# Performance work log

Measured on AMD Instinct MI355X. Metric: run time of the kernel, lower is better.

## Reference

```python
import jax, jax.numpy as jnp
import numpy as np

B, S, DIN, DOUT = 4, 2048, 2048, 8192


def setup_inputs() -> dict:
    key = jax.random.key(0)
    kx, kw = jax.random.split(key)
    x = jax.random.normal(kx, (B, S, DIN), dtype=jnp.float32)
    # match torch init: uniform(-bound, bound), bound = sqrt(3) * 0.5 * in_features**-0.5
    bound = (3.0 ** 0.5) * 0.5 * DIN ** (-0.5)
    weight = jax.random.uniform(kw, (DOUT, DIN), dtype=jnp.float32, minval=-bound, maxval=bound)
    return {"x": x, "weight": weight}


def _rms_norm(x):
    # F.rms_norm with no weight: eps defaults to finfo(dtype).eps
    eps = jnp.finfo(x.dtype).eps
    return x * jax.lax.rsqrt(jnp.mean(x * x, axis=-1, keepdims=True) + eps)


def _act_quant(xn):
    # per-token int8 symmetric quant/dequant
    scale = 127.0 / jnp.maximum(jnp.max(jnp.abs(xn), axis=-1, keepdims=True), 1e-5)
    return jnp.clip(jnp.round(xn * scale), -128.0, 127.0) / scale


def _weight_quant(w):
    # ternary weight quant/dequant with global abs-mean scale
    scale = 1.0 / jnp.maximum(jnp.mean(jnp.abs(w)), 1e-5)
    return jnp.clip(jnp.round(w * scale), -1.0, 1.0) / scale


def reference(x, weight):
    xn = _rms_norm(x)
    # STE: forward uses quantized values, gradient flows through xn / weight
    x_q = xn + jax.lax.stop_gradient(_act_quant(xn) - xn)
    w_q = weight + jax.lax.stop_gradient(_weight_quant(weight) - weight)
    # F.linear: x @ w.T  -> [B, S, DOUT]
    return jnp.einsum('bsd,od->bso', x_q, w_q)
```

## Files before the change

### kernel.cpp

```cpp
#include <hip/hip_runtime.h>

typedef unsigned short u16;
typedef unsigned int u32;
typedef int i32x4 __attribute__((ext_vector_type(4)));
typedef float f32x4 __attribute__((ext_vector_type(4)));

#define DIN 2048
#define DOUT 8192
#define MROWS 8192
#define NELEM_W (8192 * 2048)
#define NT 16

#define WS_PART 0
#define WS_WFAC 16384
#define WS_ROWFAC 16640
#define WS_XQ 49408
#define WS_WQ (49408 + 16777216)

__global__ void k_wabs(const float* __restrict__ w, double* __restrict__ part) {
    const float4* w4 = (const float4*)w;
    const unsigned t = threadIdx.x, b = blockIdx.x;
    float s = 0.f;
    for (unsigned i = b * 256u + t; i < (NELEM_W / 4); i += 2048u * 256u) {
        float4 v = w4[i];
        s += fabsf(v.x) + fabsf(v.y) + fabsf(v.z) + fabsf(v.w);
    }
    double d = (double)s;
    #pragma unroll
    for (int o = 32; o; o >>= 1) d += __shfl_down(d, o);
    __shared__ double red[4];
    if ((t & 63u) == 0u) red[t >> 6] = d;
    __syncthreads();
    if (t == 0) part[b] = red[0] + red[1] + red[2] + red[3];
}

__global__ void k_wfin(const double* __restrict__ part, float* __restrict__ wfac) {
    const int t = threadIdx.x;
    double s = 0.0;
    #pragma unroll
    for (int j = 0; j < 8; ++j) s += part[t + j * 256];
    #pragma unroll
    for (int o = 32; o; o >>= 1) s += __shfl_down(s, o);
    __shared__ double red[4];
    if ((t & 63) == 0) red[t >> 6] = s;
    __syncthreads();
    if (t == 0) {
        double mean = (red[0] + red[1] + red[2] + red[3]) * (1.0 / (double)NELEM_W);
        *wfac = fmaxf((float)mean, 1e-5f);
    }
}

__global__ void k_wquant(const float* __restrict__ w, const float* __restrict__ wfac,
                         u32* __restrict__ wq) {
    const float scale = 1.0f / *wfac;
    const float4* w4 = (const float4*)w;
    for (unsigned i = blockIdx.x * 256u + threadIdx.x; i < (NELEM_W / 4); i += 2048u * 256u) {
        float4 v = w4[i];
        int q0 = (int)fminf(fmaxf(rintf(v.x * scale), -1.f), 1.f);
        int q1 = (int)fminf(fmaxf(rintf(v.y * scale), -1.f), 1.f);
        int q2 = (int)fminf(fmaxf(rintf(v.z * scale), -1.f), 1.f);
        int q3 = (int)fminf(fmaxf(rintf(v.w * scale), -1.f), 1.f);
        wq[i] = (u32)(q0 & 255) | ((u32)(q1 & 255) << 8) |
                ((u32)(q2 & 255) << 16) | ((u32)(q3 & 255) << 24);
    }
}

__global__ void k_act(const float* __restrict__ x, u32* __restrict__ xq,
                      float* __restrict__ rowfac) {
    const int row = blockIdx.x, t = threadIdx.x;
    const float4* xr = (const float4*)(x + (size_t)row * DIN);
    float4 v0 = xr[t], v1 = xr[t + 256];
    float ss = v0.x * v0.x + v0.y * v0.y + v0.z * v0.z + v0.w * v0.w
             + v1.x * v1.x + v1.y * v1.y + v1.z * v1.z + v1.w * v1.w;
    __shared__ float red[4];
    #pragma unroll
    for (int o = 32; o; o >>= 1) ss += __shfl_down(ss, o);
    if ((t & 63) == 0) red[t >> 6] = ss;
    __syncthreads();
    ss = red[0] + red[1] + red[2] + red[3];
    const float r = 1.0f / sqrtf(ss * (1.0f / DIN) + 1.1920929e-7f);
    float xn[8] = {v0.x * r, v0.y * r, v0.z * r, v0.w * r,
                   v1.x * r, v1.y * r, v1.z * r, v1.w * r};
    float am = 0.f;
    #pragma unroll
    for (int j = 0; j < 8; ++j) am = fmaxf(am, fabsf(xn[j]));
    __syncthreads();
    #pragma unroll
    for (int o = 32; o; o >>= 1) am = fmaxf(am, __shfl_down(am, o));
    if ((t & 63) == 0) red[t >> 6] = am;
    __syncthreads();
    am = fmaxf(fmaxf(red[0], red[1]), fmaxf(red[2], red[3]));
    const float amc = fmaxf(am, 1e-5f);
    const float s = 127.0f / amc;
    int q[8];
    #pragma unroll
    for (int j = 0; j < 8; ++j)
        q[j] = (int)fminf(fmaxf(rintf(xn[j] * s), -128.f), 127.f);
    u32* xo = xq + (size_t)row * (DIN / 4);
    xo[t] = (u32)(q[0] & 255) | ((u32)(q[1] & 255) << 8) |
            ((u32)(q[2] & 255) << 16) | ((u32)(q[3] & 255) << 24);
    xo[t + 256] = (u32)(q[4] & 255) | ((u32)(q[5] & 255) << 8) |
                  ((u32)(q[6] & 255) << 16) | ((u32)(q[7] & 255) << 24);
    if (t == 0) rowfac[row] = amc * (1.0f / 127.0f);
}


#define STAGE(gbase, opOff, tt, kh) do {                                          \
    _Pragma("unroll")                                                             \
    for (int j_ = 0; j_ < 2; ++j_) {                                              \
        const int seg_ = w * 2 + j_;                                              \
        const int row_ = seg_ * 16 + (l >> 2);                                    \
        const int sc_ = (l & 3) ^ ((l >> 3) & 3);                                 \
        const char* src_ = (gbase) + (size_t)row_ * DIN + (tt) * 128 + (kh) * 64 + sc_ * 16; \
        __builtin_amdgcn_global_load_lds(                                         \
            (const __attribute__((address_space(1))) void*)src_,                  \
            (__attribute__((address_space(3))) void*)(smb + (opOff) + ((tt) & 1) * 32768 + (kh) * 16384 + seg_ * 1024), \
            16, 0, 0);                                                            \
    }                                                                             \
} while (0)

#define PHASE_MFMA(MBASE)                                                         \
    __builtin_amdgcn_s_barrier();                                                 \
    __builtin_amdgcn_s_setprio(1);                                                \
    _Pragma("unroll")                                                             \
    for (int i = 0; i < 4; ++i)                                                   \
        _Pragma("unroll")                                                         \
        for (int n = 0; n < 4; ++n)                                               \
            acc[(MBASE) + i][n] = __builtin_amdgcn_mfma_i32_16x16x64_i8(          \
                afr[i], bfr[n], acc[(MBASE) + i][n], 0, 0, 0);                    \
    __builtin_amdgcn_s_setprio(0);                                                \
    __builtin_amdgcn_s_barrier();

__launch_bounds__(512, 2)
__global__ void k_gemm(const char* __restrict__ A, const char* __restrict__ Bw,
                       const float* __restrict__ rowfac, const float* __restrict__ wfac,
                       float* __restrict__ out) {
    __shared__ __attribute__((aligned(16))) char smb[131072];

    const int t = threadIdx.x;
    const int l = t & 63, w = t >> 6;
    const int wm = w >> 2, wn = w & 3;
    const int lr = l & 15, lc = l >> 4;
    const int laneF = lr * 64 + ((lc ^ ((lr >> 1) & 3)) * 16);

    const int bid = blockIdx.x;
    const int wg = (bid & 7) * 128 + (bid >> 3);
    const int bm = wg >> 5, bn = wg & 31;

    const char* Ab = A + (size_t)(bm * 256) * DIN;
    const char* Bb = Bw + (size_t)(bn * 256) * DIN;

    i32x4 acc[8][4] = {};

    STAGE(Ab, 0, 0, 0);
    STAGE(Bb, 65536, 0, 0);
    STAGE(Ab, 0, 0, 1);
    STAGE(Bb, 65536, 0, 1);
    asm volatile("s_waitcnt vmcnt(4)" ::: "memory");
    __builtin_amdgcn_s_barrier();

    for (int kt = 0; kt < NT; ++kt) {
        const int AB = (kt & 1) * 32768;
        const bool more = (kt < NT - 1);
        const char* aBase = smb + AB;
        const char* bBase = smb + 65536 + AB;
        i32x4 afr[4], bfr[4];

        #pragma unroll
        for (int n = 0; n < 4; ++n)
            bfr[n] = *(const i32x4*)(bBase + (wn * 64 + n * 16) * 64 + laneF);
        #pragma unroll
        for (int i = 0; i < 4; ++i)
            afr[i] = *(const i32x4*)(aBase + (wm * 128 + i * 16) * 64 + laneF);
        if (more) STAGE(Ab, 0, kt + 1, 0);
        PHASE_MFMA(0)

        #pragma unroll
        for (int i = 0; i < 4; ++i)
            afr[i] = *(const i32x4*)(aBase + (wm * 128 + (4 + i) * 16) * 64 + laneF);
        if (more) {
            STAGE(Bb, 65536, kt + 1, 0);
            asm volatile("s_waitcnt vmcnt(4)" ::: "memory");
        } else {
            asm volatile("s_waitcnt vmcnt(0)" ::: "memory");
        }
        PHASE_MFMA(4)

        #pragma unroll
        for (int n = 0; n < 4; ++n)
            bfr[n] = *(const i32x4*)(bBase + 16384 + (wn * 64 + n * 16) * 64 + laneF);
        #pragma unroll
        for (int i = 0; i < 4; ++i)
            afr[i] = *(const i32x4*)(aBase + 16384 + (wm * 128 + i * 16) * 64 + laneF);
        if (more) STAGE(Ab, 0, kt + 1, 1);
        PHASE_MFMA(0)

        #pragma unroll
        for (int i = 0; i < 4; ++i)
            afr[i] = *(const i32x4*)(aBase + 16384 + (wm * 128 + (4 + i) * 16) * 64 + laneF);
        if (more) {
            STAGE(Bb, 65536, kt + 1, 1);
            asm volatile("s_waitcnt vmcnt(4)" ::: "memory");
        }
        PHASE_MFMA(4)
    }

    const float wf = *wfac;
    const int c0 = bn * 256 + wn * 64 + lr;
    #pragma unroll
    for (int m = 0; m < 8; ++m) {
        #pragma unroll
        for (int r = 0; r < 4; ++r) {
            const int grow = bm * 256 + wm * 128 + m * 16 + lc * 4 + r;
            const float s = rowfac[grow] * wf;
            const size_t ob = (size_t)grow * DOUT + c0;
            #pragma unroll
            for (int n = 0; n < 4; ++n)
                out[ob + n * 16] = (float)acc[m][n][r] * s;
        }
    }
}

extern "C" void kernel_launch(void* const* d_in, const int* in_sizes, int n_in,
                              void* d_out, int out_size, void* d_ws, size_t ws_size,
                              hipStream_t stream) {
    const float* x = (const float*)d_in[0];
    const float* wt = (const float*)d_in[1];
    float* out = (float*)d_out;
    char* ws = (char*)d_ws;

    double* part = (double*)(ws + WS_PART);
    float* wfac = (float*)(ws + WS_WFAC);
    float* rowfac = (float*)(ws + WS_ROWFAC);
    u32* xq = (u32*)(ws + WS_XQ);
    u32* wq = (u32*)(ws + WS_WQ);

    k_wabs<<<2048, 256, 0, stream>>>(wt, part);
    k_wfin<<<1, 256, 0, stream>>>(part, wfac);
    k_wquant<<<2048, 256, 0, stream>>>(wt, wfac, wq);
    k_act<<<8192, 256, 0, stream>>>(x, xq, rowfac);
    k_gemm<<<1024, 512, 0, stream>>>((const char*)xq, (const char*)wq, rowfac, wfac, out);
}
```

Before: 207.6 us.

## Restructure GEMM mainloop to full-tile double buffering and fuse quant kernels

The int8 GEMM main loop now stages a whole 128-wide K tile for A and B per step, using a new 128-byte-row XOR-swizzled LDS layout. It reads all fragments into registers before issuing 64 MFMAs, so one vmcnt(0)+barrier gate per K tile replaces the four barrier pairs per tile of the old phased loop. The weight-quant and activation-quant kernels are merged into one launch with block-index dispatch, removing a launch and letting the two run concurrently. In exchange, register pressure rises with the doubled fragment arrays, and waiting on vmcnt(0) per tile may expose load latency that the finer phasing used to hide.

```diff
diff --git a/kernel.cpp b/kernel.cpp
--- a/kernel.cpp
+++ b/kernel.cpp
@@ -3,13 +3,11 @@
 typedef unsigned short u16;
 typedef unsigned int u32;
 typedef int i32x4 __attribute__((ext_vector_type(4)));
-typedef float f32x4 __attribute__((ext_vector_type(4)));
 
 #define DIN 2048
 #define DOUT 8192
 #define MROWS 8192
 #define NELEM_W (8192 * 2048)
-#define NT 16
 
 #define WS_PART 0
 #define WS_WFAC 16384
@@ -50,24 +48,25 @@
     }
 }
 
-__global__ void k_wquant(const float* __restrict__ w, const float* __restrict__ wfac,
-                         u32* __restrict__ wq) {
-    const float scale = 1.0f / *wfac;
-    const float4* w4 = (const float4*)w;
-    for (unsigned i = blockIdx.x * 256u + threadIdx.x; i < (NELEM_W / 4); i += 2048u * 256u) {
-        float4 v = w4[i];
-        int q0 = (int)fminf(fmaxf(rintf(v.x * scale), -1.f), 1.f);
-        int q1 = (int)fminf(fmaxf(rintf(v.y * scale), -1.f), 1.f);
-        int q2 = (int)fminf(fmaxf(rintf(v.z * scale), -1.f), 1.f);
-        int q3 = (int)fminf(fmaxf(rintf(v.w * scale), -1.f), 1.f);
-        wq[i] = (u32)(q0 & 255) | ((u32)(q1 & 255) << 8) |
-                ((u32)(q2 & 255) << 16) | ((u32)(q3 & 255) << 24);
-    }
-}
-
-__global__ void k_act(const float* __restrict__ x, u32* __restrict__ xq,
-                      float* __restrict__ rowfac) {
-    const int row = blockIdx.x, t = threadIdx.x;
+__global__ void k_prep(const float* __restrict__ w, const float* __restrict__ wfac,
+                       u32* __restrict__ wq, const float* __restrict__ x,
+                       u32* __restrict__ xq, float* __restrict__ rowfac) {
+    const int t = threadIdx.x;
+    if (blockIdx.x < 2048) {
+        const float scale = 1.0f / *wfac;
+        const float4* w4 = (const float4*)w;
+        for (unsigned i = blockIdx.x * 256u + t; i < (NELEM_W / 4); i += 2048u * 256u) {
+            float4 v = w4[i];
+            int q0 = (int)fminf(fmaxf(rintf(v.x * scale), -1.f), 1.f);
+            int q1 = (int)fminf(fmaxf(rintf(v.y * scale), -1.f), 1.f);
+            int q2 = (int)fminf(fmaxf(rintf(v.z * scale), -1.f), 1.f);
+            int q3 = (int)fminf(fmaxf(rintf(v.w * scale), -1.f), 1.f);
+            wq[i] = (u32)(q0 & 255) | ((u32)(q1 & 255) << 8) |
+                    ((u32)(q2 & 255) << 16) | ((u32)(q3 & 255) << 24);
+        }
+        return;
+    }
+    const int row = blockIdx.x - 2048;
     const float4* xr = (const float4*)(x + (size_t)row * DIN);
     float4 v0 = xr[t], v1 = xr[t + 256];
     float ss = v0.x * v0.x + v0.y * v0.y + v0.z * v0.z + v0.w * v0.w
@@ -104,33 +103,6 @@
     if (t == 0) rowfac[row] = amc * (1.0f / 127.0f);
 }
 
-
-#define STAGE(gbase, opOff, tt, kh) do {                                          \
-    _Pragma("unroll")                                                             \
-    for (int j_ = 0; j_ < 2; ++j_) {                                              \
-        const int seg_ = w * 2 + j_;                                              \
-        const int row_ = seg_ * 16 + (l >> 2);                                    \
-        const int sc_ = (l & 3) ^ ((l >> 3) & 3);                                 \
-        const char* src_ = (gbase) + (size_t)row_ * DIN + (tt) * 128 + (kh) * 64 + sc_ * 16; \
-        __builtin_amdgcn_global_load_lds(                                         \
-            (const __attribute__((address_space(1))) void*)src_,                  \
-            (__attribute__((address_space(3))) void*)(smb + (opOff) + ((tt) & 1) * 32768 + (kh) * 16384 + seg_ * 1024), \
-            16, 0, 0);                                                            \
-    }                                                                             \
-} while (0)
-
-#define PHASE_MFMA(MBASE)                                                         \
-    __builtin_amdgcn_s_barrier();                                                 \
-    __builtin_amdgcn_s_setprio(1);                                                \
-    _Pragma("unroll")                                                             \
-    for (int i = 0; i < 4; ++i)                                                   \
-        _Pragma("unroll")                                                         \
-        for (int n = 0; n < 4; ++n)                                               \
-            acc[(MBASE) + i][n] = __builtin_amdgcn_mfma_i32_16x16x64_i8(          \
-                afr[i], bfr[n], acc[(MBASE) + i][n], 0, 0, 0);                    \
-    __builtin_amdgcn_s_setprio(0);                                                \
-    __builtin_amdgcn_s_barrier();
-
 __launch_bounds__(512, 2)
 __global__ void k_gemm(const char* __restrict__ A, const char* __restrict__ Bw,
                        const float* __restrict__ rowfac, const float* __restrict__ wfac,
@@ -141,69 +113,91 @@
     const int l = t & 63, w = t >> 6;
     const int wm = w >> 2, wn = w & 3;
     const int lr = l & 15, lc = l >> 4;
-    const int laneF = lr * 64 + ((lc ^ ((lr >> 1) & 3)) * 16);
+    const int swzr = lr & 7;
+    const int aB0 = (wm * 128 + lr) * 128 + ((lc ^ swzr) * 16);
+    const int aB1 = (wm * 128 + lr) * 128 + (((4 + lc) ^ swzr) * 16);
+    const int bB0 = 65536 + (wn * 64 + lr) * 128 + ((lc ^ swzr) * 16);
+    const int bB1 = 65536 + (wn * 64 + lr) * 128 + (((4 + lc) ^ swzr) * 16);
 
     const int bid = blockIdx.x;
     const int wg = (bid & 7) * 128 + (bid >> 3);
     const int bm = wg >> 5, bn = wg & 31;
-
     const char* Ab = A + (size_t)(bm * 256) * DIN;
     const char* Bb = Bw + (size_t)(bn * 256) * DIN;
 
+    const int srow = t >> 3;
+    const int loff = srow * DIN + (((t & 7) ^ (srow & 7)) * 16);
+    const int ldst = t * 16;
+
     i32x4 acc[8][4] = {};
-
-    STAGE(Ab, 0, 0, 0);
-    STAGE(Bb, 65536, 0, 0);
-    STAGE(Ab, 0, 0, 1);
-    STAGE(Bb, 65536, 0, 1);
-    asm volatile("s_waitcnt vmcnt(4)" ::: "memory");
-    __builtin_amdgcn_s_barrier();
-
-    for (int kt = 0; kt < NT; ++kt) {
-        const int AB = (kt & 1) * 32768;
-        const bool more = (kt < NT - 1);
-        const char* aBase = smb + AB;
-        const char* bBase = smb + 65536 + AB;
-        i32x4 afr[4], bfr[4];
-
-        #pragma unroll
-        for (int n = 0; n < 4; ++n)
-            bfr[n] = *(const i32x4*)(bBase + (wn * 64 + n * 16) * 64 + laneF);
-        #pragma unroll
-        for (int i = 0; i < 4; ++i)
-            afr[i] = *(const i32x4*)(aBase + (wm * 128 + i * 16) * 64 + laneF);
-        if (more) STAGE(Ab, 0, kt + 1, 0);
-        PHASE_MFMA(0)
-
-        #pragma unroll
-        for (int i = 0; i < 4; ++i)
-            afr[i] = *(const i32x4*)(aBase + (wm * 128 + (4 + i) * 16) * 64 + laneF);
-        if (more) {
-            STAGE(Bb, 65536, kt + 1, 0);
-            asm volatile("s_waitcnt vmcnt(4)" ::: "memory");
-        } else {
-            asm volatile("s_waitcnt vmcnt(0)" ::: "memory");
-        }
-        PHASE_MFMA(4)
-
-        #pragma unroll
-        for (int n = 0; n < 4; ++n)
-            bfr[n] = *(const i32x4*)(bBase + 16384 + (wn * 64 + n * 16) * 64 + laneF);
-        #pragma unroll
-        for (int i = 0; i < 4; ++i)
-            afr[i] = *(const i32x4*)(aBase + 16384 + (wm * 128 + i * 16) * 64 + laneF);
-        if (more) STAGE(Ab, 0, kt + 1, 1);
-        PHASE_MFMA(0)
-
-        #pragma unroll
-        for (int i = 0; i < 4; ++i)
-            afr[i] = *(const i32x4*)(aBase + 16384 + (wm * 128 + (4 + i) * 16) * 64 + laneF);
-        if (more) {
-            STAGE(Bb, 65536, kt + 1, 1);
-            asm volatile("s_waitcnt vmcnt(4)" ::: "memory");
-        }
-        PHASE_MFMA(4)
-    }
+    i32x4 fa[2][8], fb[2][4];
+
+#define STG(ktB, s) do {                                                          \
+    _Pragma("unroll")                                                             \
+    for (int j_ = 0; j_ < 4; ++j_)                                                \
+        __builtin_amdgcn_global_load_lds(                                         \
+            (const __attribute__((address_space(1))) void*)(Ab + (size_t)(j_ * 64) * DIN + loff + (ktB)), \
+            (__attribute__((address_space(3))) void*)(smb + (s) * 32768 + j_ * 8192 + ldst), 16, 0, 0); \
+    _Pragma("unroll")                                                             \
+    for (int j_ = 0; j_ < 4; ++j_)                                                \
+        __builtin_amdgcn_global_load_lds(                                         \
+            (const __attribute__((address_space(1))) void*)(Bb + (size_t)(j_ * 64) * DIN + loff + (ktB)), \
+            (__attribute__((address_space(3))) void*)(smb + 65536 + (s) * 32768 + j_ * 8192 + ldst), 16, 0, 0); \
+} while (0)
+
+#define RDA(s) do {                                                               \
+    _Pragma("unroll")                                                             \
+    for (int m_ = 0; m_ < 8; ++m_) {                                              \
+        fa[0][m_] = *(const i32x4*)(smb + (s) * 32768 + aB0 + m_ * 2048);         \
+        fa[1][m_] = *(const i32x4*)(smb + (s) * 32768 + aB1 + m_ * 2048);         \
+    }                                                                             \
+    _Pragma("unroll")                                                             \
+    for (int n_ = 0; n_ < 4; ++n_) {                                              \
+        fb[0][n_] = *(const i32x4*)(smb + (s) * 32768 + bB0 + n_ * 2048);         \
+        fb[1][n_] = *(const i32x4*)(smb + (s) * 32768 + bB1 + n_ * 2048);         \
+    }                                                                             \
+} while (0)
+
+#define MFM() do {                                                                \
+    __builtin_amdgcn_s_setprio(1);                                                \
+    _Pragma("unroll")                                                             \
+    for (int kh_ = 0; kh_ < 2; ++kh_)                                             \
+        _Pragma("unroll")                                                         \
+        for (int m_ = 0; m_ < 8; ++m_)                                            \
+            _Pragma("unroll")                                                     \
+            for (int n_ = 0; n_ < 4; ++n_)                                        \
+                acc[m_][n_] = __builtin_amdgcn_mfma_i32_16x16x64_i8(              \
+                    fa[kh_][m_], fb[kh_][n_], acc[m_][n_], 0, 0, 0);              \
+    __builtin_amdgcn_s_setprio(0);                                                \
+} while (0)
+
+#define GATE() do {                                                               \
+    asm volatile("s_waitcnt vmcnt(0)" ::: "memory");                              \
+    __builtin_amdgcn_s_barrier();                                                 \
+} while (0)
+
+    STG(0, 0);
+    GATE();
+    RDA(0);
+
+    int kb = 128;
+    #pragma unroll 1
+    for (int pair = 0; pair < 7; ++pair) {
+        STG(kb, 1);
+        MFM();
+        GATE();
+        RDA(1);
+        STG(kb + 128, 0);
+        MFM();
+        GATE();
+        RDA(0);
+        kb += 256;
+    }
+    STG(kb, 1);
+    MFM();
+    GATE();
+    RDA(1);
+    MFM();
 
     const float wf = *wfac;
     const int c0 = bn * 256 + wn * 64 + lr;
@@ -219,6 +213,10 @@
                 out[ob + n * 16] = (float)acc[m][n][r] * s;
         }
     }
+#undef STG
+#undef RDA
+#undef MFM
+#undef GATE
 }
 
 extern "C" void kernel_launch(void* const* d_in, const int* in_sizes, int n_in,
@@ -237,7 +235,6 @@
 
     k_wabs<<<2048, 256, 0, stream>>>(wt, part);
     k_wfin<<<1, 256, 0, stream>>>(part, wfac);
-    k_wquant<<<2048, 256, 0, stream>>>(wt, wfac, wq);
-    k_act<<<8192, 256, 0, stream>>>(x, xq, rowfac);
+    k_prep<<<2048 + MROWS, 256, 0, stream>>>(wt, wfac, wq, x, xq, rowfac);
     k_gemm<<<1024, 512, 0, stream>>>((const char*)xq, (const char*)wq, rowfac, wfac, out);
 }
```

After: 203.8 us. Within noise of the previous version (-1.8%).

## Merge quant kernels and make GEMM persistent over 2x2 tile groups

Applied to the files above, without the earlier changes.

Merges the weight-quant and activation-quant kernels into one launch, with block ranges dispatched by block index, to remove a launch and let the two overlap. The GEMM now launches 256 blocks, one per CU at two blocks per CU, and each block loops over four 256x256 output tiles in a 2x2 group mapped per XCD. This aims to cut tail effects and improve L2 reuse of A and B panels. In exchange, the pipeline prologue is restarted per tile with no overlap between tiles, and the epilogue stores are serialized with the next tile's loads.

```diff
diff --git a/kernel.cpp b/kernel.cpp
--- a/kernel.cpp
+++ b/kernel.cpp
@@ -1,9 +1,7 @@
 #include <hip/hip_runtime.h>
 
-typedef unsigned short u16;
 typedef unsigned int u32;
 typedef int i32x4 __attribute__((ext_vector_type(4)));
-typedef float f32x4 __attribute__((ext_vector_type(4)));
 
 #define DIN 2048
 #define DOUT 8192
@@ -50,24 +48,25 @@
     }
 }
 
-__global__ void k_wquant(const float* __restrict__ w, const float* __restrict__ wfac,
-                         u32* __restrict__ wq) {
-    const float scale = 1.0f / *wfac;
-    const float4* w4 = (const float4*)w;
-    for (unsigned i = blockIdx.x * 256u + threadIdx.x; i < (NELEM_W / 4); i += 2048u * 256u) {
-        float4 v = w4[i];
-        int q0 = (int)fminf(fmaxf(rintf(v.x * scale), -1.f), 1.f);
-        int q1 = (int)fminf(fmaxf(rintf(v.y * scale), -1.f), 1.f);
-        int q2 = (int)fminf(fmaxf(rintf(v.z * scale), -1.f), 1.f);
-        int q3 = (int)fminf(fmaxf(rintf(v.w * scale), -1.f), 1.f);
-        wq[i] = (u32)(q0 & 255) | ((u32)(q1 & 255) << 8) |
-                ((u32)(q2 & 255) << 16) | ((u32)(q3 & 255) << 24);
-    }
-}
-
-__global__ void k_act(const float* __restrict__ x, u32* __restrict__ xq,
-                      float* __restrict__ rowfac) {
-    const int row = blockIdx.x, t = threadIdx.x;
+__global__ void k_prep(const float* __restrict__ w, const float* __restrict__ wfac,
+                       u32* __restrict__ wq, const float* __restrict__ x,
+                       u32* __restrict__ xq, float* __restrict__ rowfac) {
+    const int t = threadIdx.x;
+    if (blockIdx.x < 2048) {
+        const float scale = 1.0f / *wfac;
+        const float4* w4 = (const float4*)w;
+        for (unsigned i = blockIdx.x * 256u + t; i < (NELEM_W / 4); i += 2048u * 256u) {
+            float4 v = w4[i];
+            int q0 = (int)fminf(fmaxf(rintf(v.x * scale), -1.f), 1.f);
+            int q1 = (int)fminf(fmaxf(rintf(v.y * scale), -1.f), 1.f);
+            int q2 = (int)fminf(fmaxf(rintf(v.z * scale), -1.f), 1.f);
+            int q3 = (int)fminf(fmaxf(rintf(v.w * scale), -1.f), 1.f);
+            wq[i] = (u32)(q0 & 255) | ((u32)(q1 & 255) << 8) |
+                    ((u32)(q2 & 255) << 16) | ((u32)(q3 & 255) << 24);
+        }
+        return;
+    }
+    const int row = blockIdx.x - 2048;
     const float4* xr = (const float4*)(x + (size_t)row * DIN);
     float4 v0 = xr[t], v1 = xr[t + 256];
     float ss = v0.x * v0.x + v0.y * v0.y + v0.z * v0.z + v0.w * v0.w
@@ -104,6 +103,24 @@
     if (t == 0) rowfac[row] = amc * (1.0f / 127.0f);
 }
 
+__launch_bounds__(512, 2)
+__global__ void k_gemm(const char* __restrict__ A, const char* __restrict__ Bw,
+                       const float* __restrict__ rowfac, const float* __restrict__ wfac,
+                       float* __restrict__ out) {
+    __shared__ __attribute__((aligned(16))) char smb[131072];
+
+    const int t = threadIdx.x;
+    const int l = t & 63, w = t >> 6;
+    const int wm = w >> 2, wn = w & 3;
+    const int lr = l & 15, lc = l >> 4;
+    const int laneF = lr * 64 + ((lc ^ ((lr >> 1) & 3)) * 16);
+
+    const int bid = blockIdx.x;
+    const int xcd = bid & 7, idx = bid >> 3;
+    const int st = xcd * 32 + idx;
+    const int sm = st >> 4, sn = st & 15;
+
+    const float wf = *wfac;
 
 #define STAGE(gbase, opOff, tt, kh) do {                                          \
     _Pragma("unroll")                                                             \
@@ -131,94 +148,85 @@
     __builtin_amdgcn_s_setprio(0);                                                \
     __builtin_amdgcn_s_barrier();
 
-__launch_bounds__(512, 2)
-__global__ void k_gemm(const char* __restrict__ A, const char* __restrict__ Bw,
-                       const float* __restrict__ rowfac, const float* __restrict__ wfac,
-                       float* __restrict__ out) {
-    __shared__ __attribute__((aligned(16))) char smb[131072];
-
-    const int t = threadIdx.x;
-    const int l = t & 63, w = t >> 6;
-    const int wm = w >> 2, wn = w & 3;
-    const int lr = l & 15, lc = l >> 4;
-    const int laneF = lr * 64 + ((lc ^ ((lr >> 1) & 3)) * 16);
-
-    const int bid = blockIdx.x;
-    const int wg = (bid & 7) * 128 + (bid >> 3);
-    const int bm = wg >> 5, bn = wg & 31;
-
-    const char* Ab = A + (size_t)(bm * 256) * DIN;
-    const char* Bb = Bw + (size_t)(bn * 256) * DIN;
-
-    i32x4 acc[8][4] = {};
-
-    STAGE(Ab, 0, 0, 0);
-    STAGE(Bb, 65536, 0, 0);
-    STAGE(Ab, 0, 0, 1);
-    STAGE(Bb, 65536, 0, 1);
-    asm volatile("s_waitcnt vmcnt(4)" ::: "memory");
-    __builtin_amdgcn_s_barrier();
-
-    for (int kt = 0; kt < NT; ++kt) {
-        const int AB = (kt & 1) * 32768;
-        const bool more = (kt < NT - 1);
-        const char* aBase = smb + AB;
-        const char* bBase = smb + 65536 + AB;
-        i32x4 afr[4], bfr[4];
-
+    #pragma unroll 1
+    for (int j = 0; j < 4; ++j) {
+        const int bm = sm * 2 + (j >> 1);
+        const int bn = sn * 2 + ((j & 1) ^ (j >> 1));
+        const char* Ab = A + (size_t)(bm * 256) * DIN;
+        const char* Bb = Bw + (size_t)(bn * 256) * DIN;
+
+        i32x4 acc[8][4] = {};
+
+        STAGE(Ab, 0,     0, 0);
+        STAGE(Bb, 65536, 0, 0);
+        STAGE(Ab, 0,     0, 1);
+        STAGE(Bb, 65536, 0, 1);
+        asm volatile("s_waitcnt vmcnt(4)" ::: "memory");
+        __builtin_amdgcn_s_barrier();
+
+        #pragma unroll 1
+        for (int kt = 0; kt < NT; ++kt) {
+            const int AB = (kt & 1) * 32768;
+            const bool more = (kt < NT - 1);
+            const char* aBase = smb + AB;
+            const char* bBase = smb + 65536 + AB;
+            i32x4 afr[4], bfr[4];
+
+            #pragma unroll
+            for (int n = 0; n < 4; ++n)
+                bfr[n] = *(const i32x4*)(bBase + (wn * 64 + n * 16) * 64 + laneF);
+            #pragma unroll
+            for (int i = 0; i < 4; ++i)
+                afr[i] = *(const i32x4*)(aBase + (wm * 128 + i * 16) * 64 + laneF);
+            if (more) STAGE(Ab, 0, kt + 1, 0);
+            PHASE_MFMA(0)
+
+            #pragma unroll
+            for (int i = 0; i < 4; ++i)
+                afr[i] = *(const i32x4*)(aBase + (wm * 128 + (4 + i) * 16) * 64 + laneF);
+            if (more) {
+                STAGE(Bb, 65536, kt + 1, 0);
+                asm volatile("s_waitcnt vmcnt(4)" ::: "memory");
+            } else {
+                asm volatile("s_waitcnt vmcnt(0)" ::: "memory");
+            }
+            PHASE_MFMA(4)
+
+            #pragma unroll
+            for (int n = 0; n < 4; ++n)
+                bfr[n] = *(const i32x4*)(bBase + 16384 + (wn * 64 + n * 16) * 64 + laneF);
+            #pragma unroll
+            for (int i = 0; i < 4; ++i)
+                afr[i] = *(const i32x4*)(aBase + 16384 + (wm * 128 + i * 16) * 64 + laneF);
+            if (more) STAGE(Ab, 0, kt + 1, 1);
+            PHASE_MFMA(0)
+
+            #pragma unroll
+            for (int i = 0; i < 4; ++i)
+                afr[i] = *(const i32x4*)(aBase + 16384 + (wm * 128 + (4 + i) * 16) * 64 + laneF);
+            if (more) {
+                STAGE(Bb, 65536, kt + 1, 1);
+                asm volatile("s_waitcnt vmcnt(4)" ::: "memory");
+            }
+            PHASE_MFMA(4)
+        }
+
+        const int c0 = bn * 256 + wn * 64 + lr;
         #pragma unroll
-        for (int n = 0; n < 4; ++n)
-            bfr[n] = *(const i32x4*)(bBase + (wn * 64 + n * 16) * 64 + laneF);
-        #pragma unroll
-        for (int i = 0; i < 4; ++i)
-            afr[i] = *(const i32x4*)(aBase + (wm * 128 + i * 16) * 64 + laneF);
-        if (more) STAGE(Ab, 0, kt + 1, 0);
-        PHASE_MFMA(0)
-
-        #pragma unroll
-        for (int i = 0; i < 4; ++i)
-            afr[i] = *(const i32x4*)(aBase + (wm * 128 + (4 + i) * 16) * 64 + laneF);
-        if (more) {
-            STAGE(Bb, 65536, kt + 1, 0);
-            asm volatile("s_waitcnt vmcnt(4)" ::: "memory");
-        } else {
-            asm volatile("s_waitcnt vmcnt(0)" ::: "memory");
+        for (int m = 0; m < 8; ++m) {
+            #pragma unroll
+            for (int r = 0; r < 4; ++r) {
+                const int grow = bm * 256 + wm * 128 + m * 16 + lc * 4 + r;
+                const float s = rowfac[grow] * wf;
+                const size_t ob = (size_t)grow * DOUT + c0;
+                #pragma unroll
+                for (int n = 0; n < 4; ++n)
+                    out[ob + n * 16] = (float)acc[m][n][r] * s;
+            }
         }
-        PHASE_MFMA(4)
-
-        #pragma unroll
-        for (int n = 0; n < 4; ++n)
-            bfr[n] = *(const i32x4*)(bBase + 16384 + (wn * 64 + n * 16) * 64 + laneF);
-        #pragma unroll
-        for (int i = 0; i < 4; ++i)
-            afr[i] = *(const i32x4*)(aBase + 16384 + (wm * 128 + i * 16) * 64 + laneF);
-        if (more) STAGE(Ab, 0, kt + 1, 1);
-        PHASE_MFMA(0)
-
-        #pragma unroll
-        for (int i = 0; i < 4; ++i)
-            afr[i] = *(const i32x4*)(aBase + 16384 + (wm * 128 + (4 + i) * 16) * 64 + laneF);
-        if (more) {
-            STAGE(Bb, 65536, kt + 1, 1);
-            asm volatile("s_waitcnt vmcnt(4)" ::: "memory");
-        }
-        PHASE_MFMA(4)
-    }
-
-    const float wf = *wfac;
-    const int c0 = bn * 256 + wn * 64 + lr;
-    #pragma unroll
-    for (int m = 0; m < 8; ++m) {
-        #pragma unroll
-        for (int r = 0; r < 4; ++r) {
-            const int grow = bm * 256 + wm * 128 + m * 16 + lc * 4 + r;
-            const float s = rowfac[grow] * wf;
-            const size_t ob = (size_t)grow * DOUT + c0;
-            #pragma unroll
-            for (int n = 0; n < 4; ++n)
-                out[ob + n * 16] = (float)acc[m][n][r] * s;
-        }
-    }
+    }
+#undef STAGE
+#undef PHASE_MFMA
 }
 
 extern "C" void kernel_launch(void* const* d_in, const int* in_sizes, int n_in,
@@ -237,7 +245,6 @@
 
     k_wabs<<<2048, 256, 0, stream>>>(wt, part);
     k_wfin<<<1, 256, 0, stream>>>(part, wfac);
-    k_wquant<<<2048, 256, 0, stream>>>(wt, wfac, wq);
-    k_act<<<8192, 256, 0, stream>>>(x, xq, rowfac);
-    k_gemm<<<1024, 512, 0, stream>>>((const char*)xq, (const char*)wq, rowfac, wfac, out);
-}
+    k_prep<<<2048 + MROWS, 256, 0, stream>>>(wt, wfac, wq, x, xq, rowfac);
+    k_gemm<<<256, 512, 0, stream>>>((const char*)xq, (const char*)wq, rowfac, wfac, out);
+}
```

After: 210.1 us. No clear change (+1.2%).
